# Optimization experiments

Measured on AMD Instinct MI355X. Metric: run time of the kernel, lower is better.

The kernel has to match this reference:

```python
import jax, jax.numpy as jnp
import numpy as np

B, L, D = 4, 1536, 768
H, DQK, DV = 8, 64, 96
NPF = 96  # num_pos_feats = (DV // (2*3)) * (2*3)


def pos_feats_exponential(positions, feature_size, seq_length, min_half_life=3.0):
    # positions: (P, 1); returns (P, feature_size)
    max_range = jnp.log(seq_length) / jnp.log(2.0)
    half_life = jnp.power(2.0, jnp.linspace(min_half_life, max_range, feature_size))
    return jnp.exp(-jnp.log(2.0) / half_life * jnp.abs(positions))


def pos_feats_central_mask(positions, feature_size):
    center_widths = jnp.power(2.0, jnp.arange(1, feature_size + 1, dtype=jnp.float32)) - 1.0
    return (center_widths > jnp.abs(positions)).astype(jnp.float32)


def pos_feats_gamma(positions, feature_size, seq_length):
    stddev = seq_length / (2.0 * feature_size)
    start_mean = seq_length / feature_size
    mean = jnp.linspace(start_mean, seq_length, feature_size)
    concentration = (mean / stddev) ** 2
    rate = mean / (stddev ** 2)
    x = jnp.abs(positions)
    log_unnorm = jax.scipy.special.xlogy(concentration - 1.0, x) - rate * x
    log_norm = jax.scipy.special.gammaln(concentration) - concentration * jnp.log(rate)
    probs = jnp.exp(log_unnorm - log_norm) + 1e-8
    return probs / jnp.max(probs, axis=0, keepdims=True)


def pos_feats_all(positions, feature_size, seq_length, symmetric=False):
    # 3 feature functions; if asymmetric, each is doubled by a signed copy
    num_basis = feature_size // 6
    emb = jnp.concatenate([
        pos_feats_exponential(positions, num_basis, seq_length),
        pos_feats_central_mask(positions, num_basis),
        pos_feats_gamma(positions, num_basis, seq_length),
    ], axis=-1)
    if not symmetric:
        emb = jnp.concatenate([emb, jnp.sign(positions) * emb], axis=-1)
    return emb  # (P, feature_size)


def relative_shift(x):
    # x: (b, h, t1, 2*t1 - 1) -> (b, h, t1, t1), Transformer-XL shift trick
    b, h, t1, t2 = x.shape
    x = jnp.concatenate([jnp.zeros_like(x[..., :1]), x], axis=-1)  # pad -> width t2+1 == 2*t1
    x = x.reshape(b, h, t2 + 1, t1)[:, :, 1:, :]
    x = x.reshape(b, h, t1, t2)
    return x[..., : (t2 + 2) // 2]


def setup_inputs() -> dict:
    key = jax.random.key(0)
    ks = jax.random.split(key, 9)

    def vs(k, shape):  # VarianceScaling(scale=2.0), fan_in on leading dim for 2D
        fan_in = shape[0] if len(shape) == 2 else shape[-1]
        return jax.random.normal(k, shape, jnp.float32) * np.float32(np.sqrt(2.0 / fan_in))

    return {
        "x": jax.random.normal(ks[0], (B, L, D), jnp.float32),
        "Q_w": vs(ks[1], (D, H * DQK)),
        "K_w": vs(ks[2], (D, H * DQK)),
        "V_w": vs(ks[3], (D, H * DV)),
        "out_w": vs(ks[4], (D, H * DV)),
        "out_b": jnp.zeros((H * DV,), jnp.float32),
        "rel_K_w": vs(ks[5], (NPF, H * DQK)),
        "r_w_bias": vs(ks[6], (1, H, 1, DQK)),
        "r_r_bias": vs(ks[7], (1, H, 1, DQK)),
    }


def reference(x, Q_w, K_w, V_w, out_w, out_b, rel_K_w, r_w_bias, r_r_bias):
    b, l, d = x.shape
    h = r_w_bias.shape[1]
    dqk = Q_w.shape[1] // h

    def heads(w, inp):
        out = inp @ w  # (b, t, h*dh)
        return out.reshape(inp.shape[0], inp.shape[1], h, -1).transpose(0, 2, 1, 3)

    Q = heads(Q_w, x) * (dqk ** -0.5)  # scaling=True
    K = heads(K_w, x)
    V = heads(V_w, x)

    positions = jnp.arange(1 - l, l, dtype=jnp.float32)[:, None]       # (2l-1, 1)
    pe = pos_feats_all(positions, rel_K_w.shape[0], float(l))           # (2l-1, npf)
    r_K = (pe @ rel_K_w).reshape(2 * l - 1, h, dqk).transpose(1, 0, 2)  # (h, 2l-1, dqk)

    content = jnp.einsum('bhid,bhjd->bhij', Q + r_w_bias, K)            # (b, h, l, l)
    rel = jnp.einsum('bhid,hjd->bhij', Q + r_r_bias, r_K)               # (b, h, l, 2l-1)
    logits = content + relative_shift(rel)

    w = jax.nn.softmax(logits, axis=-1)
    attn = jnp.einsum('bhij,bhjd->bhid', w, V)                          # (b, h, l, dv)
    out = attn.transpose(0, 2, 1, 3).reshape(b, l, -1) @ out_w + out_b
    return out
```

## Files before the change

### kernel.cpp

```cpp
#include <hip/hip_runtime.h>


typedef unsigned short u16;
typedef unsigned int   u32;

typedef __bf16 bf16x8_t __attribute__((ext_vector_type(8)));
typedef unsigned short u16x8_t __attribute__((ext_vector_type(8)));
typedef float f32x4_t __attribute__((ext_vector_type(4)));

union Frag { u16x8_t u; bf16x8_t b; };

__device__ __forceinline__ float bf2f(u16 v){
  union { u32 i; float f; } c; c.i = ((u32)v) << 16; return c.f;
}
__device__ __forceinline__ u16 f2bf(float f){
  union { float f; u32 i; } c; c.f = f;
  u32 r = c.i + 0x7FFFu + ((c.i >> 16) & 1u);
  return (u16)(r >> 16);
}

#define GLB __attribute__((address_space(1)))
#define LDSAS __attribute__((address_space(3)))
__device__ __forceinline__ void async16(const void* g, void* l){
  __builtin_amdgcn_global_load_lds((const GLB u32*)g, (LDSAS u32*)l, 16, 0, 0);
}

#define LQ   1536
#define NPOS 3071
#define NPOSP 3072

__global__ void cvt_x(const float* __restrict__ x, u16* __restrict__ xb)
{
  int gid = blockIdx.x * 256 + threadIdx.x;
  float4 v = ((const float4*)x)[gid];
  xb[4*gid+0] = f2bf(v.x); xb[4*gid+1] = f2bf(v.y);
  xb[4*gid+2] = f2bf(v.z); xb[4*gid+3] = f2bf(v.w);
}

__global__ __launch_bounds__(256) void transpose_w(
    const float* __restrict__ Qw_, const float* __restrict__ Kw_,
    const float* __restrict__ Vw_, const float* __restrict__ Ow_,
    u16* __restrict__ WtQKV, u16* __restrict__ WtOut)
{
  __shared__ u16 tile[64][65];
  int bx = blockIdx.x;
  const float* src; int stride, cl0, c0, k0; u16* dst;
  if (bx < 336) {
    int ct = bx % 28, kt = bx / 28;
    c0 = ct*64; k0 = kt*64;
    if (c0 < 512)       { src = Qw_; stride = 512; cl0 = c0; }
    else if (c0 < 1024) { src = Kw_; stride = 512; cl0 = c0 - 512; }
    else                { src = Vw_; stride = 768; cl0 = c0 - 1024; }
    dst = WtQKV;
  } else {
    int b2 = bx - 336; int ct = b2 % 12, kt = b2 / 12;
    c0 = ct*64; k0 = kt*64; src = Ow_; stride = 768; cl0 = c0; dst = WtOut;
  }
  int t = threadIdx.x;
  #pragma unroll
  for (int e = 0; e < 16; ++e) {
    int idx = e*256 + t; int row = idx >> 6, col = idx & 63;
    tile[row][col] = f2bf(src[(size_t)(k0 + row)*stride + cl0 + col]);
  }
  __syncthreads();
  #pragma unroll
  for (int e = 0; e < 16; ++e) {
    int idx = e*256 + t; int orow = idx >> 6, ocol = idx & 63;
    dst[(size_t)(c0 + orow)*768 + k0 + ocol] = tile[ocol][orow];
  }
}

__global__ void gamma_max_k(float* __restrict__ gmax)
{
  int f = blockIdx.x;
  float fi   = (float)(f + 1);
  float conc = 4.0f * fi * fi;
  float rate = fi / 24.0f;
  float c1   = conc - 1.0f;
  float lognorm = lgammaf(conc) - conc * logf(rate);
  float mx = 0.0f;
  for (int x = threadIdx.x; x < 1536; x += 256) {
    float xf = (float)x;
    float lu = (x == 0) ? -INFINITY : (c1 * logf(xf) - rate * xf);
    float p  = expf(lu - lognorm) + 1e-8f;
    mx = fmaxf(mx, p);
  }
  for (int d = 1; d < 64; d <<= 1) mx = fmaxf(mx, __shfl_xor(mx, d, 64));
  __shared__ float red[4];
  if ((threadIdx.x & 63) == 0) red[threadIdx.x >> 6] = mx;
  __syncthreads();
  if (threadIdx.x == 0)
    gmax[f] = fmaxf(fmaxf(red[0], red[1]), fmaxf(red[2], red[3]));
}

__global__ void rk_k(const float* __restrict__ gmax,
                     const float* __restrict__ relKw, u16* __restrict__ rK)
{
  int k = blockIdx.x;
  int t = threadIdx.x;
  if (k == NPOS) {
    for (int c = t; c < 512; c += 256)
      rK[(((size_t)(c >> 6))*NPOSP + NPOS)*64 + (c & 63)] = 0;
    return;
  }
  __shared__ float feats[96];
  float pos = (float)(k - (LQ - 1));
  float x   = fabsf(pos);
  float sgn = (float)((pos > 0.0f) - (pos < 0.0f));
  if (t < 96) {
    int tb = (t < 48) ? t : t - 48;
    float val;
    if (tb < 16) {
      float max_range = log2f((float)LQ);
      float hl = exp2f(3.0f + (float)tb * (max_range - 3.0f) / 15.0f);
      val = expf(-0.69314718056f / hl * x);
    } else if (tb < 32) {
      int i = tb - 16;
      float width = (float)(1u << (i + 1)) - 1.0f;
      val = (width > x) ? 1.0f : 0.0f;
    } else {
      int i = tb - 32;
      float fi   = (float)(i + 1);
      float conc = 4.0f * fi * fi;
      float rate = fi / 24.0f;
      float lognorm = lgammaf(conc) - conc * logf(rate);
      float lu = (x == 0.0f) ? -INFINITY : ((conc - 1.0f) * logf(x) - rate * x);
      float p  = expf(lu - lognorm) + 1e-8f;
      val = p / gmax[i];
    }
    feats[t] = (t < 48) ? val : sgn * val;
  }
  __syncthreads();
  for (int c = t; c < 512; c += 256) {
    float acc = 0.0f;
    #pragma unroll 8
    for (int f = 0; f < 96; ++f) acc += feats[f] * relKw[(size_t)f*512 + c];
    rK[(((size_t)(c >> 6))*NPOSP + k)*64 + (c & 63)] = f2bf(acc);
  }
}

__global__ __launch_bounds__(256) void qkv_gemm(
    const u16* __restrict__ xb, const u16* __restrict__ Wt,
    u16* __restrict__ Qb, u16* __restrict__ Kc, u16* __restrict__ Vt)
{
  const int n0 = blockIdx.x * 64;
  const int m0 = blockIdx.y * 64;
  const int tid = threadIdx.x, w = tid >> 6, lane = tid & 63, q = lane >> 4, s = lane & 15;

  __shared__ __align__(16) u16 At[64*64];
  __shared__ __align__(16) u16 Bt[64*64];

  const char* ag = (const char*)(xb + (size_t)m0 * 768);
  const char* bg = (const char*)(Wt + (size_t)n0 * 768);

  const f32x4_t fz = {0.f, 0.f, 0.f, 0.f};
  f32x4_t acc[4] = {fz, fz, fz, fz};

  for (int kk = 0; kk < 768; kk += 64) {
    #pragma unroll
    for (int c = 0; c < 2; ++c) {
      int ck = w*128 + c*64 + lane;
      int grow = ck >> 3, gcol = (ck & 7) ^ (grow & 7);
      async16(ag + (size_t)grow*1536 + (size_t)(kk + gcol*8)*2, &At[(size_t)(w*128 + c*64)*8]);
      async16(bg + (size_t)grow*1536 + (size_t)(kk + gcol*8)*2, &Bt[(size_t)(w*128 + c*64)*8]);
    }
    __syncthreads();
    #pragma unroll
    for (int kf = 0; kf < 2; ++kf) {
      int sw = (kf*4 + q) ^ (s & 7);
      Frag af; af.u = *(const u16x8_t*)&At[(size_t)((16*w + s)*8 + sw)*8];
      #pragma unroll
      for (int ns = 0; ns < 4; ++ns) {
        Frag bf; bf.u = *(const u16x8_t*)&Bt[(size_t)((ns*16 + s)*8 + sw)*8];
        acc[ns] = __builtin_amdgcn_mfma_f32_16x16x32_bf16(af.b, bf.b, acc[ns], 0, 0, 0);
      }
    }
    __syncthreads();
  }

  #pragma unroll
  for (int ns = 0; ns < 4; ++ns) {
    int c = n0 + ns*16 + s;
    #pragma unroll
    for (int r = 0; r < 4; ++r) {
      int row = m0 + 16*w + q*4 + r;
      int b = row / LQ, i = row - b*LQ;
      float v = acc[ns][r];
      if (c < 512) {
        int h = c >> 6, d = c & 63;
        Qb[(((size_t)(b*8 + h))*LQ + i)*64 + d] = f2bf(v * 0.125f);
      } else if (c < 1024) {
        int cc = c - 512, h = cc >> 6, d = cc & 63;
        Kc[(((size_t)(b*8 + h))*LQ + i)*64 + d] = f2bf(v);
      } else {
        int cc = c - 1024, h = cc / 96, vv = cc - h*96;
        Vt[(((size_t)(b*8 + h))*96 + vv)*LQ + i] = f2bf(v);
      }
    }
  }
}

__global__ __launch_bounds__(512, 4) void attn_k(
    const u16* __restrict__ Qb, const u16* __restrict__ Kc,
    const u16* __restrict__ Vt, const u16* __restrict__ rK,
    const float* __restrict__ rwb, const float* __restrict__ rrb,
    u16* __restrict__ attnO, u16* __restrict__ Opart, float* __restrict__ ml,
    int nz)
{
  const int n = blockIdx.x;
  const int bpb = 12 * nz;
  const int slot = n >> 3;
  const int bh = (n & 7) * 4 + slot / bpb;
  const int rm = slot % bpb;
  const int it = rm % 12, z = rm / 12;
  const int i0 = it * 128;
  const int b = bh >> 3, h = bh & 7;
  const int tid = threadIdx.x;
  const int w = tid >> 6, lane = tid & 63, q = lane >> 4, s = lane & 15;

  __shared__ __align__(16) u16 Kt[64*64];
  __shared__ __align__(16) u16 Rt[256*64];
  __shared__ __align__(16) u16 Vs[96*64];
  __shared__ __align__(16) u16 Ps[8][16][72];

  Frag qwf[2], qrf[2];
  {
    const u16* qb = Qb + (((size_t)bh)*LQ + i0 + 16*w + s)*64;
    #pragma unroll
    for (int kf = 0; kf < 2; ++kf) {
      u16x8_t qraw = *(const u16x8_t*)(qb + kf*32 + q*8);
      #pragma unroll
      for (int j = 0; j < 8; ++j) {
        int d = kf*32 + q*8 + j;
        float qv = bf2f(qraw[j]);
        qwf[kf].u[j] = f2bf(qv + rwb[h*64 + d]);
        qrf[kf].u[j] = f2bf(qv + rrb[h*64 + d]);
      }
    }
  }

  Frag ones;
  #pragma unroll
  for (int j = 0; j < 8; ++j) ones.u[j] = 0x3F80;

  const f32x4_t fz = {0.f, 0.f, 0.f, 0.f};
  float mrun[4];
  f32x4_t acco[6], accl;
  #pragma unroll
  for (int r = 0; r < 4; ++r) mrun[r] = -1e30f;
  #pragma unroll
  for (int vs = 0; vs < 6; ++vs) acco[vs] = fz;
  accl = fz;

  const char* kcb = (const char*)(Kc + ((size_t)bh)*LQ*64);
  const char* vtb = (const char*)(Vt + ((size_t)bh)*96*LQ);
  const char* rkb = (const char*)(rK + ((size_t)h)*NPOSP*64);

  const int swz0 = (0*4 + q) ^ (s & 7);
  const int swz1 = (1*4 + q) ^ (s & 7);

  const int njt = 24 / nz;
  const int jt0 = z * njt;
  const int jtend = jt0 + njt;

  auto stageK = [&](int jtS) {
    const char* kg = kcb + (size_t)(jtS*64) * 128;
    int ck = tid;
    int grow = ck >> 3, gcol = (ck & 7) ^ (grow & 7);
    async16(kg + (size_t)grow*128 + gcol*16, &Kt[(size_t)(w*64)*8]);
  };
  auto stageV = [&](int jtS) {
    const char* vg = vtb + (size_t)(jtS*64) * 2;
    {
      int ck = tid;
      int grow = ck >> 3, gcol = (ck & 7) ^ (grow & 7);
      async16(vg + (size_t)grow*(LQ*2) + gcol*16, &Vs[(size_t)(w*64)*8]);
    }
    if (tid < 256) {
      int ck = 512 + tid;
      int grow = ck >> 3, gcol = (ck & 7) ^ (grow & 7);
      async16(vg + (size_t)grow*(LQ*2) + gcol*16, &Vs[(size_t)(512 + w*64)*8]);
    }
  };
  auto stageR64 = [&](int ar0) {
    const char* rg = rkb + (size_t)ar0 * 128;
    int ck = tid;
    int grow = ck >> 3, gcol = (ck & 7) ^ (grow & 7);
    async16(rg + (size_t)grow*128 + gcol*16, &Rt[(size_t)((ar0 & 255) + w*8)*64]);
  };

  {
    const int k00 = jt0*64 - i0 + (LQ - 128);
    stageK(jt0);
    stageR64(k00); stageR64(k00 + 64); stageR64(k00 + 128);
    stageV(jt0);
  }
  __syncthreads();

  for (int jt = jt0; jt < jtend; ++jt) {
    const int k0 = jt*64 - i0 + (LQ - 128);
    const int kb = k0 & 255;

    f32x4_t accc[4] = {fz, fz, fz, fz};
    #pragma unroll
    for (int ns = 0; ns < 4; ++ns) {
      int row = ns*16 + s;
      Frag b0; b0.u = *(const u16x8_t*)&Kt[(size_t)(row*8 + swz0)*8];
      Frag b1; b1.u = *(const u16x8_t*)&Kt[(size_t)(row*8 + swz1)*8];
      accc[ns] = __builtin_amdgcn_mfma_f32_16x16x32_bf16(qwf[0].b, b0.b, accc[ns], 0, 0, 0);
      accc[ns] = __builtin_amdgcn_mfma_f32_16x16x32_bf16(qwf[1].b, b1.b, accc[ns], 0, 0, 0);
    }

    f32x4_t accr[5] = {fz, fz, fz, fz, fz};
    #pragma unroll
    for (int nn = 0; nn < 5; ++nn) {
      int row = (kb + (7 - w + nn)*16 + s) & 255;
      Frag b0; b0.u = *(const u16x8_t*)&Rt[(size_t)(row*8 + swz0)*8];
      Frag b1; b1.u = *(const u16x8_t*)&Rt[(size_t)(row*8 + swz1)*8];
      accr[nn] = __builtin_amdgcn_mfma_f32_16x16x32_bf16(qrf[0].b, b0.b, accr[nn], 0, 0, 0);
      accr[nn] = __builtin_amdgcn_mfma_f32_16x16x32_bf16(qrf[1].b, b1.b, accr[nn], 0, 0, 0);
    }

    __syncthreads();

    if (jt + 1 < jtend) {
      stageK(jt + 1);
      stageR64(k0 + 192);
    }

    #pragma unroll
    for (int r = 0; r < 4; ++r) {
      int tt = s + 15 - 4*q - r;
      int srcl = (lane & 48) | (tt & 15);
      bool hi = tt >= 16;
      float v[5];
      #pragma unroll
      for (int nn = 0; nn < 5; ++nn) v[nn] = __shfl(accr[nn][r], srcl, 64);
      #pragma unroll
      for (int ns = 0; ns < 4; ++ns)
        accc[ns][r] += hi ? v[ns + 1] : v[ns];
    }

    #pragma unroll
    for (int r = 0; r < 4; ++r) {
      float mx = fmaxf(fmaxf(accc[0][r], accc[1][r]), fmaxf(accc[2][r], accc[3][r]));
      for (int d = 1; d < 16; d <<= 1) mx = fmaxf(mx, __shfl_xor(mx, d, 64));
      float mnew  = fmaxf(mrun[r], mx);
      float alpha = __expf(mrun[r] - mnew);
      #pragma unroll
      for (int ns = 0; ns < 4; ++ns)
        accc[ns][r] = __expf(accc[ns][r] - mnew);
      mrun[r] = mnew;
      accl[r] *= alpha;
      #pragma unroll
      for (int vs = 0; vs < 6; ++vs) acco[vs][r] *= alpha;
    }

    #pragma unroll
    for (int ns = 0; ns < 4; ++ns)
      #pragma unroll
      for (int r = 0; r < 4; ++r)
        Ps[w][q*4 + r][ns*16 + s] = f2bf(accc[ns][r]);

    #pragma unroll
    for (int kf = 0; kf < 2; ++kf) {
      Frag pf; pf.u = *(const u16x8_t*)(&Ps[w][s][kf*32 + q*8]);
      int sw = kf ? swz1 : swz0;
      #pragma unroll
      for (int vs = 0; vs < 6; ++vs) {
        int row = vs*16 + s;
        Frag vf; vf.u = *(const u16x8_t*)&Vs[(size_t)(row*8 + sw)*8];
        acco[vs] = __builtin_amdgcn_mfma_f32_16x16x32_bf16(pf.b, vf.b, acco[vs], 0, 0, 0);
      }
      accl = __builtin_amdgcn_mfma_f32_16x16x32_bf16(pf.b, ones.b, accl, 0, 0, 0);
    }

    __syncthreads();

    if (jt + 1 < jtend) stageV(jt + 1);
  }

  if (nz == 1) {
    #pragma unroll
    for (int vs = 0; vs < 6; ++vs) {
      int v = vs*16 + s;
      #pragma unroll
      for (int r = 0; r < 4; ++r) {
        int i = i0 + 16*w + q*4 + r;
        attnO[((size_t)b*LQ + i)*768 + h*96 + v] = f2bf(acco[vs][r] / accl[r]);
      }
    }
  } else {
    #pragma unroll
    for (int vs = 0; vs < 6; ++vs) {
      int v = vs*16 + s;
      #pragma unroll
      for (int r = 0; r < 4; ++r) {
        int i = i0 + 16*w + q*4 + r;
        size_t rg = (size_t)(z*32 + bh)*LQ + i;
        Opart[rg*96 + v] = f2bf(acco[vs][r]);
      }
    }
    if (s == 0) {
      #pragma unroll
      for (int r = 0; r < 4; ++r) {
        int i = i0 + 16*w + q*4 + r;
        size_t rg = (size_t)(z*32 + bh)*LQ + i;
        ml[rg*2 + 0] = mrun[r];
        ml[rg*2 + 1] = accl[r];
      }
    }
  }
}

__global__ void combine_k(const u16* __restrict__ Opart, const float* __restrict__ ml,
                          u16* __restrict__ attnO, int nz)
{
  int g = blockIdx.x * 256 + threadIdx.x;
  if (g >= 32*LQ*96) return;
  int v = g % 96, row = g / 96;
  int bh = row / LQ, i = row - bh*LQ;
  int b = bh >> 3, h = bh & 7;
  float M = -1e30f;
  for (int z = 0; z < nz; ++z)
    M = fmaxf(M, ml[((size_t)(z*32 + bh)*LQ + i)*2]);
  float L = 0.f, num = 0.f;
  for (int z = 0; z < nz; ++z) {
    size_t rg = (size_t)(z*32 + bh)*LQ + i;
    float e = __expf(ml[rg*2] - M);
    L   += ml[rg*2 + 1] * e;
    num += bf2f(Opart[rg*96 + v]) * e;
  }
  attnO[((size_t)b*LQ + i)*768 + h*96 + v] = f2bf(num / L);
}

__global__ __launch_bounds__(256) void out_gemm(
    const u16* __restrict__ A, const u16* __restrict__ Wt,
    const float* __restrict__ bias, float* __restrict__ out)
{
  const int n0 = blockIdx.x * 64;
  const int m0 = blockIdx.y * 64;
  const int tid = threadIdx.x, w = tid >> 6, lane = tid & 63, q = lane >> 4, s = lane & 15;

  __shared__ __align__(16) u16 At[64*64];
  __shared__ __align__(16) u16 Bt[64*64];

  const char* ag = (const char*)(A  + (size_t)m0 * 768);
  const char* bg = (const char*)(Wt + (size_t)n0 * 768);

  const f32x4_t fz = {0.f, 0.f, 0.f, 0.f};
  f32x4_t acc[4] = {fz, fz, fz, fz};

  for (int kk = 0; kk < 768; kk += 64) {
    #pragma unroll
    for (int c = 0; c < 2; ++c) {
      int ck = w*128 + c*64 + lane;
      int grow = ck >> 3, gcol = (ck & 7) ^ (grow & 7);
      async16(ag + (size_t)grow*1536 + (size_t)(kk + gcol*8)*2, &At[(size_t)(w*128 + c*64)*8]);
      async16(bg + (size_t)grow*1536 + (size_t)(kk + gcol*8)*2, &Bt[(size_t)(w*128 + c*64)*8]);
    }
    __syncthreads();
    #pragma unroll
    for (int kf = 0; kf < 2; ++kf) {
      int sw = (kf*4 + q) ^ (s & 7);
      Frag af; af.u = *(const u16x8_t*)&At[(size_t)((16*w + s)*8 + sw)*8];
      #pragma unroll
      for (int ns = 0; ns < 4; ++ns) {
        Frag bf; bf.u = *(const u16x8_t*)&Bt[(size_t)((ns*16 + s)*8 + sw)*8];
        acc[ns] = __builtin_amdgcn_mfma_f32_16x16x32_bf16(af.b, bf.b, acc[ns], 0, 0, 0);
      }
    }
    __syncthreads();
  }

  #pragma unroll
  for (int ns = 0; ns < 4; ++ns) {
    int c = n0 + ns*16 + s;
    float bv = bias[c];
    #pragma unroll
    for (int r = 0; r < 4; ++r) {
      int row = m0 + 16*w + q*4 + r;
      out[(size_t)row*768 + c] = acc[ns][r] + bv;
    }
  }
}

extern "C" void kernel_launch(void* const* d_in, const int* in_sizes, int n_in,
                              void* d_out, int out_size, void* d_ws, size_t ws_size,
                              hipStream_t stream)
{
  (void)out_size;

  static const int dict_sig[9] = {4718592,393216,393216,589824,589824,768,49152,512,512};
  bool is_dict = (n_in == 9);
  for (int i = 0; i < 9 && i < n_in; ++i)
    if (in_sizes[i] != dict_sig[i]) is_dict = false;

  const float *x, *Qw_w, *Kw_w, *Vw_w, *Ow_w, *out_b, *relKw, *rwb, *rrb;
  if (is_dict) {
    x     = (const float*)d_in[0];  Qw_w  = (const float*)d_in[1];
    Kw_w  = (const float*)d_in[2];  Vw_w  = (const float*)d_in[3];
    Ow_w  = (const float*)d_in[4];  out_b = (const float*)d_in[5];
    relKw = (const float*)d_in[6];  rwb   = (const float*)d_in[7];
    rrb   = (const float*)d_in[8];
  } else {
    const float* p393[2] = {nullptr,nullptr}; int n393 = 0;
    const float* p589[2] = {nullptr,nullptr}; int n589 = 0;
    const float* p512[2] = {nullptr,nullptr}; int n512 = 0;
    const float *px = nullptr, *prel = nullptr, *pb = nullptr;
    for (int i = 0; i < n_in; ++i) {
      const float* p = (const float*)d_in[i];
      switch (in_sizes[i]) {
        case 4718592: px = p; break;
        case 49152:   prel = p; break;
        case 768:     pb = p; break;
        case 393216:  if (n393 < 2) p393[n393++] = p; break;
        case 589824:  if (n589 < 2) p589[n589++] = p; break;
        case 512:     if (n512 < 2) p512[n512++] = p; break;
        default: break;
      }
    }
    x = px; relKw = prel; out_b = pb;
    Qw_w = p393[0]; Kw_w = p393[1];
    Vw_w = p589[0]; Ow_w = p589[1];
    rwb  = p512[0]; rrb  = p512[1];
  }

  float* out = (float*)d_out;

  char* ws = (char*)d_ws;
  size_t off = 0;
  auto alloc = [&](size_t bytes) -> void* {
    void* p = ws + off;
    off += (bytes + 255) & ~(size_t)255;
    return p;
  };

  float* gmax  = (float*)alloc(256);
  u16*   WtQKV = (u16*)  alloc((size_t)1792*768*2);
  u16*   WtOut = (u16*)  alloc((size_t)768*768*2);
  u16*   rK    = (u16*)  alloc((size_t)8*NPOSP*64*2);
  u16*   Qb    = (u16*)  alloc((size_t)32*LQ*64*2);
  u16*   Kc    = (u16*)  alloc((size_t)32*LQ*64*2);
  u16*   Vt    = (u16*)  alloc((size_t)32*96*LQ*2);
  u16*   xb    = (u16*)  alloc((size_t)6144*768*2);
  u16*   attnO = xb;

  size_t base_off = off;
  auto need = [&](int nzv) -> size_t {
    size_t o = base_off;
    o += (((size_t)nzv*32*LQ*96*2) + 255) & ~(size_t)255;
    o += (((size_t)nzv*32*LQ*2*4) + 255) & ~(size_t)255;
    return o;
  };
  int nz = 1;
  if (ws_size >= need(4)) nz = 4;
  else if (ws_size >= need(2)) nz = 2;
  u16*   Opart = nullptr; float* ml = nullptr;
  if (nz > 1) {
    Opart = (u16*)  alloc((size_t)nz*32*LQ*96*2);
    ml    = (float*)alloc((size_t)nz*32*LQ*2*4);
  }

  cvt_x      <<<dim3(4608), dim3(256), 0, stream>>>(x, xb);
  transpose_w<<<dim3(480),  dim3(256), 0, stream>>>(Qw_w, Kw_w, Vw_w, Ow_w, WtQKV, WtOut);
  gamma_max_k<<<dim3(16),   dim3(256), 0, stream>>>(gmax);
  rk_k       <<<dim3(NPOSP),dim3(256), 0, stream>>>(gmax, relKw, rK);
  qkv_gemm   <<<dim3(28,96),dim3(256), 0, stream>>>(xb, WtQKV, Qb, Kc, Vt);
  attn_k     <<<dim3(384*nz),dim3(512), 0, stream>>>(Qb, Kc, Vt, rK, rwb, rrb,
                                                     attnO, Opart, ml, nz);
  if (nz > 1)
    combine_k<<<dim3(18432), dim3(256), 0, stream>>>(Opart, ml, attnO, nz);
  out_gemm   <<<dim3(12,96),dim3(256), 0, stream>>>(attnO, WtOut, out_b, out);
}
```

Measured before the change: 328.4 us.

## Enlarge GEMM tiles, batch rK positions per block, use hardware bf16 conversion

The QKV GEMM moves to 128x128 tiles with 4x4 MFMA fragments per wave, and the output GEMM to 128x64 tiles. Both changes raise data reuse per LDS load and reduce block count. The rK kernel now computes four positions per block so each relKw weight load is reused four times. The attention kernel uses the hardware bf16 conversion and raises wave priority (s_setprio) around its MFMA sections. Larger tiles lower occupancy and shrink the grid, and the hardware conversion may round differently from the manual routine.

```diff
diff --git a/kernel.cpp b/kernel.cpp
--- a/kernel.cpp
+++ b/kernel.cpp
@@ -17,6 +17,10 @@
   union { float f; u32 i; } c; c.f = f;
   u32 r = c.i + 0x7FFFu + ((c.i >> 16) & 1u);
   return (u16)(r >> 16);
+}
+__device__ __forceinline__ u16 f2bf_hw(float f){
+  __bf16 h = (__bf16)f;
+  union { __bf16 h; u16 u; } c; c.h = h; return c.u;
 }
 
 #define GLB __attribute__((address_space(1)))
@@ -93,49 +97,68 @@
     gmax[f] = fmaxf(fmaxf(red[0], red[1]), fmaxf(red[2], red[3]));
 }
 
-__global__ void rk_k(const float* __restrict__ gmax,
+__global__ __launch_bounds__(256) void rk_k(const float* __restrict__ gmax,
                      const float* __restrict__ relKw, u16* __restrict__ rK)
 {
-  int k = blockIdx.x;
-  int t = threadIdx.x;
-  if (k == NPOS) {
-    for (int c = t; c < 512; c += 256)
-      rK[(((size_t)(c >> 6))*NPOSP + NPOS)*64 + (c & 63)] = 0;
-    return;
-  }
-  __shared__ float feats[96];
-  float pos = (float)(k - (LQ - 1));
-  float x   = fabsf(pos);
-  float sgn = (float)((pos > 0.0f) - (pos < 0.0f));
-  if (t < 96) {
-    int tb = (t < 48) ? t : t - 48;
-    float val;
-    if (tb < 16) {
-      float max_range = log2f((float)LQ);
-      float hl = exp2f(3.0f + (float)tb * (max_range - 3.0f) / 15.0f);
-      val = expf(-0.69314718056f / hl * x);
-    } else if (tb < 32) {
-      int i = tb - 16;
-      float width = (float)(1u << (i + 1)) - 1.0f;
-      val = (width > x) ? 1.0f : 0.0f;
-    } else {
-      int i = tb - 32;
-      float fi   = (float)(i + 1);
-      float conc = 4.0f * fi * fi;
-      float rate = fi / 24.0f;
-      float lognorm = lgammaf(conc) - conc * logf(rate);
-      float lu = (x == 0.0f) ? -INFINITY : ((conc - 1.0f) * logf(x) - rate * x);
-      float p  = expf(lu - lognorm) + 1e-8f;
-      val = p / gmax[i];
-    }
-    feats[t] = (t < 48) ? val : sgn * val;
+  __shared__ float feats[4][96];
+  const int k0 = blockIdx.x * 4;
+  const int t = threadIdx.x;
+
+  #pragma unroll
+  for (int e = 0; e < 2; ++e) {
+    int idx = e*256 + t;
+    if (idx < 384) {
+      int kl = idx / 96, f = idx - kl*96;
+      int k = k0 + kl;
+      float val = 0.0f;
+      if (k != NPOS) {
+        float pos = (float)(k - (LQ - 1));
+        float x   = fabsf(pos);
+        float sgn = (float)((pos > 0.0f) - (pos < 0.0f));
+        int fb = (f < 48) ? f : f - 48;
+        float v;
+        if (fb < 16) {
+          float max_range = log2f((float)LQ);
+          float hl = exp2f(3.0f + (float)fb * (max_range - 3.0f) / 15.0f);
+          v = expf(-0.69314718056f / hl * x);
+        } else if (fb < 32) {
+          int i = fb - 16;
+          float width = (float)(1u << (i + 1)) - 1.0f;
+          v = (width > x) ? 1.0f : 0.0f;
+        } else {
+          int i = fb - 32;
+          float fi   = (float)(i + 1);
+          float conc = 4.0f * fi * fi;
+          float rate = fi / 24.0f;
+          float lognorm = lgammaf(conc) - conc * logf(rate);
+          float lu = (x == 0.0f) ? -INFINITY : ((conc - 1.0f) * logf(x) - rate * x);
+          float p  = expf(lu - lognorm) + 1e-8f;
+          v = p / gmax[i];
+        }
+        val = (f < 48) ? v : sgn * v;
+      }
+      feats[kl][f] = val;
+    }
   }
   __syncthreads();
-  for (int c = t; c < 512; c += 256) {
-    float acc = 0.0f;
-    #pragma unroll 8
-    for (int f = 0; f < 96; ++f) acc += feats[f] * relKw[(size_t)f*512 + c];
-    rK[(((size_t)(c >> 6))*NPOSP + k)*64 + (c & 63)] = f2bf(acc);
+
+  #pragma unroll
+  for (int ci = 0; ci < 2; ++ci) {
+    int c = ci*256 + t;
+    float a0 = 0.f, a1 = 0.f, a2 = 0.f, a3 = 0.f;
+    #pragma unroll 4
+    for (int f = 0; f < 96; ++f) {
+      float wv = relKw[(size_t)f*512 + c];
+      a0 += feats[0][f] * wv;
+      a1 += feats[1][f] * wv;
+      a2 += feats[2][f] * wv;
+      a3 += feats[3][f] * wv;
+    }
+    size_t base = (((size_t)(c >> 6))*NPOSP + k0)*64 + (c & 63);
+    rK[base +   0] = f2bf(a0);
+    rK[base +  64] = f2bf(a1);
+    rK[base + 128] = f2bf(a2);
+    rK[base + 192] = f2bf(a3);
   }
 }
 
@@ -143,58 +166,72 @@
     const u16* __restrict__ xb, const u16* __restrict__ Wt,
     u16* __restrict__ Qb, u16* __restrict__ Kc, u16* __restrict__ Vt)
 {
-  const int n0 = blockIdx.x * 64;
-  const int m0 = blockIdx.y * 64;
+  const int n0 = blockIdx.x * 128;
+  const int m0 = blockIdx.y * 128;
   const int tid = threadIdx.x, w = tid >> 6, lane = tid & 63, q = lane >> 4, s = lane & 15;
-
-  __shared__ __align__(16) u16 At[64*64];
-  __shared__ __align__(16) u16 Bt[64*64];
+  const int wr = w >> 1, wc = w & 1;
+
+  __shared__ __align__(16) u16 At[128*64];
+  __shared__ __align__(16) u16 Bt[128*64];
 
   const char* ag = (const char*)(xb + (size_t)m0 * 768);
   const char* bg = (const char*)(Wt + (size_t)n0 * 768);
 
   const f32x4_t fz = {0.f, 0.f, 0.f, 0.f};
-  f32x4_t acc[4] = {fz, fz, fz, fz};
+  f32x4_t acc[4][4];
+  #pragma unroll
+  for (int m = 0; m < 4; ++m)
+    #pragma unroll
+    for (int n = 0; n < 4; ++n) acc[m][n] = fz;
 
   for (int kk = 0; kk < 768; kk += 64) {
     #pragma unroll
-    for (int c = 0; c < 2; ++c) {
-      int ck = w*128 + c*64 + lane;
+    for (int c = 0; c < 4; ++c) {
+      int ck = w*256 + c*64 + lane;
       int grow = ck >> 3, gcol = (ck & 7) ^ (grow & 7);
-      async16(ag + (size_t)grow*1536 + (size_t)(kk + gcol*8)*2, &At[(size_t)(w*128 + c*64)*8]);
-      async16(bg + (size_t)grow*1536 + (size_t)(kk + gcol*8)*2, &Bt[(size_t)(w*128 + c*64)*8]);
+      async16(ag + (size_t)grow*1536 + (size_t)(kk + gcol*8)*2, &At[(size_t)(w*256 + c*64)*8]);
+      async16(bg + (size_t)grow*1536 + (size_t)(kk + gcol*8)*2, &Bt[(size_t)(w*256 + c*64)*8]);
     }
     __syncthreads();
     #pragma unroll
     for (int kf = 0; kf < 2; ++kf) {
       int sw = (kf*4 + q) ^ (s & 7);
-      Frag af; af.u = *(const u16x8_t*)&At[(size_t)((16*w + s)*8 + sw)*8];
-      #pragma unroll
-      for (int ns = 0; ns < 4; ++ns) {
-        Frag bf; bf.u = *(const u16x8_t*)&Bt[(size_t)((ns*16 + s)*8 + sw)*8];
-        acc[ns] = __builtin_amdgcn_mfma_f32_16x16x32_bf16(af.b, bf.b, acc[ns], 0, 0, 0);
-      }
+      Frag af[4], bf[4];
+      #pragma unroll
+      for (int m = 0; m < 4; ++m)
+        af[m].u = *(const u16x8_t*)&At[(size_t)((wr*64 + m*16 + s)*8 + sw)*8];
+      #pragma unroll
+      for (int n = 0; n < 4; ++n)
+        bf[n].u = *(const u16x8_t*)&Bt[(size_t)((wc*64 + n*16 + s)*8 + sw)*8];
+      #pragma unroll
+      for (int m = 0; m < 4; ++m)
+        #pragma unroll
+        for (int n = 0; n < 4; ++n)
+          acc[m][n] = __builtin_amdgcn_mfma_f32_16x16x32_bf16(af[m].b, bf[n].b, acc[m][n], 0, 0, 0);
     }
     __syncthreads();
   }
 
   #pragma unroll
-  for (int ns = 0; ns < 4; ++ns) {
-    int c = n0 + ns*16 + s;
-    #pragma unroll
-    for (int r = 0; r < 4; ++r) {
-      int row = m0 + 16*w + q*4 + r;
-      int b = row / LQ, i = row - b*LQ;
-      float v = acc[ns][r];
-      if (c < 512) {
-        int h = c >> 6, d = c & 63;
-        Qb[(((size_t)(b*8 + h))*LQ + i)*64 + d] = f2bf(v * 0.125f);
-      } else if (c < 1024) {
-        int cc = c - 512, h = cc >> 6, d = cc & 63;
-        Kc[(((size_t)(b*8 + h))*LQ + i)*64 + d] = f2bf(v);
-      } else {
-        int cc = c - 1024, h = cc / 96, vv = cc - h*96;
-        Vt[(((size_t)(b*8 + h))*96 + vv)*LQ + i] = f2bf(v);
+  for (int m = 0; m < 4; ++m) {
+    #pragma unroll
+    for (int n = 0; n < 4; ++n) {
+      int c = n0 + wc*64 + n*16 + s;
+      #pragma unroll
+      for (int r = 0; r < 4; ++r) {
+        int row = m0 + wr*64 + m*16 + q*4 + r;
+        int b = row / LQ, i = row - b*LQ;
+        float v = acc[m][n][r];
+        if (c < 512) {
+          int h = c >> 6, d = c & 63;
+          Qb[(((size_t)(b*8 + h))*LQ + i)*64 + d] = f2bf(v * 0.125f);
+        } else if (c < 1024) {
+          int cc = c - 512, h = cc >> 6, d = cc & 63;
+          Kc[(((size_t)(b*8 + h))*LQ + i)*64 + d] = f2bf(v);
+        } else {
+          int cc = c - 1024, h = cc / 96, vv = cc - h*96;
+          Vt[(((size_t)(b*8 + h))*96 + vv)*LQ + i] = f2bf(v);
+        }
       }
     }
   }
@@ -233,8 +270,8 @@
       for (int j = 0; j < 8; ++j) {
         int d = kf*32 + q*8 + j;
         float qv = bf2f(qraw[j]);
-        qwf[kf].u[j] = f2bf(qv + rwb[h*64 + d]);
-        qrf[kf].u[j] = f2bf(qv + rrb[h*64 + d]);
+        qwf[kf].u[j] = f2bf_hw(qv + rwb[h*64 + d]);
+        qrf[kf].u[j] = f2bf_hw(qv + rrb[h*64 + d]);
       }
     }
   }
@@ -302,6 +339,8 @@
     const int kb = k0 & 255;
 
     f32x4_t accc[4] = {fz, fz, fz, fz};
+    f32x4_t accr[5] = {fz, fz, fz, fz, fz};
+    __builtin_amdgcn_s_setprio(1);
     #pragma unroll
     for (int ns = 0; ns < 4; ++ns) {
       int row = ns*16 + s;
@@ -310,8 +349,6 @@
       accc[ns] = __builtin_amdgcn_mfma_f32_16x16x32_bf16(qwf[0].b, b0.b, accc[ns], 0, 0, 0);
       accc[ns] = __builtin_amdgcn_mfma_f32_16x16x32_bf16(qwf[1].b, b1.b, accc[ns], 0, 0, 0);
     }
-
-    f32x4_t accr[5] = {fz, fz, fz, fz, fz};
     #pragma unroll
     for (int nn = 0; nn < 5; ++nn) {
       int row = (kb + (7 - w + nn)*16 + s) & 255;
@@ -320,6 +357,7 @@
       accr[nn] = __builtin_amdgcn_mfma_f32_16x16x32_bf16(qrf[0].b, b0.b, accr[nn], 0, 0, 0);
       accr[nn] = __builtin_amdgcn_mfma_f32_16x16x32_bf16(qrf[1].b, b1.b, accr[nn], 0, 0, 0);
     }
+    __builtin_amdgcn_s_setprio(0);
 
     __syncthreads();
 
@@ -360,8 +398,9 @@
     for (int ns = 0; ns < 4; ++ns)
       #pragma unroll
       for (int r = 0; r < 4; ++r)
-        Ps[w][q*4 + r][ns*16 + s] = f2bf(accc[ns][r]);
-
+        Ps[w][q*4 + r][ns*16 + s] = f2bf_hw(accc[ns][r]);
+
+    __builtin_amdgcn_s_setprio(1);
     #pragma unroll
     for (int kf = 0; kf < 2; ++kf) {
       Frag pf; pf.u = *(const u16x8_t*)(&Ps[w][s][kf*32 + q*8]);
@@ -374,6 +413,7 @@
       }
       accl = __builtin_amdgcn_mfma_f32_16x16x32_bf16(pf.b, ones.b, accl, 0, 0, 0);
     }
+    __builtin_amdgcn_s_setprio(0);
 
     __syncthreads();
 
@@ -387,7 +427,7 @@
       #pragma unroll
       for (int r = 0; r < 4; ++r) {
         int i = i0 + 16*w + q*4 + r;
-        attnO[((size_t)b*LQ + i)*768 + h*96 + v] = f2bf(acco[vs][r] / accl[r]);
+        attnO[((size_t)b*LQ + i)*768 + h*96 + v] = f2bf_hw(acco[vs][r] / accl[r]);
       }
     }
   } else {
@@ -398,7 +438,7 @@
       for (int r = 0; r < 4; ++r) {
         int i = i0 + 16*w + q*4 + r;
         size_t rg = (size_t)(z*32 + bh)*LQ + i;
-        Opart[rg*96 + v] = f2bf(acco[vs][r]);
+        Opart[rg*96 + v] = f2bf_hw(acco[vs][r]);
       }
     }
     if (s == 0) {
@@ -439,48 +479,66 @@
     const float* __restrict__ bias, float* __restrict__ out)
 {
   const int n0 = blockIdx.x * 64;
-  const int m0 = blockIdx.y * 64;
+  const int m0 = blockIdx.y * 128;
   const int tid = threadIdx.x, w = tid >> 6, lane = tid & 63, q = lane >> 4, s = lane & 15;
 
-  __shared__ __align__(16) u16 At[64*64];
+  __shared__ __align__(16) u16 At[128*64];
   __shared__ __align__(16) u16 Bt[64*64];
 
   const char* ag = (const char*)(A  + (size_t)m0 * 768);
   const char* bg = (const char*)(Wt + (size_t)n0 * 768);
 
   const f32x4_t fz = {0.f, 0.f, 0.f, 0.f};
-  f32x4_t acc[4] = {fz, fz, fz, fz};
+  f32x4_t acc[2][4];
+  #pragma unroll
+  for (int m = 0; m < 2; ++m)
+    #pragma unroll
+    for (int n = 0; n < 4; ++n) acc[m][n] = fz;
 
   for (int kk = 0; kk < 768; kk += 64) {
+    #pragma unroll
+    for (int c = 0; c < 4; ++c) {
+      int ck = w*256 + c*64 + lane;
+      int grow = ck >> 3, gcol = (ck & 7) ^ (grow & 7);
+      async16(ag + (size_t)grow*1536 + (size_t)(kk + gcol*8)*2, &At[(size_t)(w*256 + c*64)*8]);
+    }
     #pragma unroll
     for (int c = 0; c < 2; ++c) {
       int ck = w*128 + c*64 + lane;
       int grow = ck >> 3, gcol = (ck & 7) ^ (grow & 7);
-      async16(ag + (size_t)grow*1536 + (size_t)(kk + gcol*8)*2, &At[(size_t)(w*128 + c*64)*8]);
       async16(bg + (size_t)grow*1536 + (size_t)(kk + gcol*8)*2, &Bt[(size_t)(w*128 + c*64)*8]);
     }
     __syncthreads();
     #pragma unroll
     for (int kf = 0; kf < 2; ++kf) {
       int sw = (kf*4 + q) ^ (s & 7);
-      Frag af; af.u = *(const u16x8_t*)&At[(size_t)((16*w + s)*8 + sw)*8];
-      #pragma unroll
-      for (int ns = 0; ns < 4; ++ns) {
-        Frag bf; bf.u = *(const u16x8_t*)&Bt[(size_t)((ns*16 + s)*8 + sw)*8];
-        acc[ns] = __builtin_amdgcn_mfma_f32_16x16x32_bf16(af.b, bf.b, acc[ns], 0, 0, 0);
-      }
+      Frag af[2], bf[4];
+      #pragma unroll
+      for (int m = 0; m < 2; ++m)
+        af[m].u = *(const u16x8_t*)&At[(size_t)((w*32 + m*16 + s)*8 + sw)*8];
+      #pragma unroll
+      for (int n = 0; n < 4; ++n)
+        bf[n].u = *(const u16x8_t*)&Bt[(size_t)((n*16 + s)*8 + sw)*8];
+      #pragma unroll
+      for (int m = 0; m < 2; ++m)
+        #pragma unroll
+        for (int n = 0; n < 4; ++n)
+          acc[m][n] = __builtin_amdgcn_mfma_f32_16x16x32_bf16(af[m].b, bf[n].b, acc[m][n], 0, 0, 0);
     }
     __syncthreads();
   }
 
   #pragma unroll
-  for (int ns = 0; ns < 4; ++ns) {
-    int c = n0 + ns*16 + s;
-    float bv = bias[c];
-    #pragma unroll
-    for (int r = 0; r < 4; ++r) {
-      int row = m0 + 16*w + q*4 + r;
-      out[(size_t)row*768 + c] = acc[ns][r] + bv;
+  for (int m = 0; m < 2; ++m) {
+    #pragma unroll
+    for (int n = 0; n < 4; ++n) {
+      int c = n0 + n*16 + s;
+      float bv = bias[c];
+      #pragma unroll
+      for (int r = 0; r < 4; ++r) {
+        int row = m0 + w*32 + m*16 + q*4 + r;
+        out[(size_t)row*768 + c] = acc[m][n][r] + bv;
+      }
     }
   }
 }
@@ -565,11 +623,11 @@
   cvt_x      <<<dim3(4608), dim3(256), 0, stream>>>(x, xb);
   transpose_w<<<dim3(480),  dim3(256), 0, stream>>>(Qw_w, Kw_w, Vw_w, Ow_w, WtQKV, WtOut);
   gamma_max_k<<<dim3(16),   dim3(256), 0, stream>>>(gmax);
-  rk_k       <<<dim3(NPOSP),dim3(256), 0, stream>>>(gmax, relKw, rK);
-  qkv_gemm   <<<dim3(28,96),dim3(256), 0, stream>>>(xb, WtQKV, Qb, Kc, Vt);
+  rk_k       <<<dim3(768),  dim3(256), 0, stream>>>(gmax, relKw, rK);
+  qkv_gemm   <<<dim3(14,48),dim3(256), 0, stream>>>(xb, WtQKV, Qb, Kc, Vt);
   attn_k     <<<dim3(384*nz),dim3(512), 0, stream>>>(Qb, Kc, Vt, rK, rwb, rrb,
                                                      attnO, Opart, ml, nz);
   if (nz > 1)
     combine_k<<<dim3(18432), dim3(256), 0, stream>>>(Opart, ml, attnO, nz);
-  out_gemm   <<<dim3(12,96),dim3(256), 0, stream>>>(attnO, WtOut, out_b, out);
-}
+  out_gemm   <<<dim3(12,48),dim3(256), 0, stream>>>(attnO, WtOut, out_b, out);
+}
```

New measurement: 349.9 us. 1.07x slower.

## Fuse preprocessing kernels and streamline online softmax with exp2 and lazy rescale

Applied to the files above, without the earlier changes.

Merges the x conversion, weight transposes, gamma-max and relative-key feature kernels into one launch. The gamma max is now taken analytically from the distribution mode rather than by scanning every position, and each block computes four positions so relKw loads are shared. In attention, Q is prescaled by log2(e) so exp2 replaces exp, and the row max uses DPP row rotations instead of shuffles. The softmax rescale is skipped when no row max rises more than a threshold above the running max, and hardware bf16 conversion plus a reciprocal replace software rounding and division. These changes can alter rounding slightly, and the lazy rescale allows larger intermediate values in the accumulators.

```diff
diff --git a/kernel.cpp b/kernel.cpp
--- a/kernel.cpp
+++ b/kernel.cpp
@@ -18,6 +18,32 @@
   u32 r = c.i + 0x7FFFu + ((c.i >> 16) & 1u);
   return (u16)(r >> 16);
 }
+__device__ __forceinline__ u16 f2bf_hw(float f){
+  __bf16 h = (__bf16)f;
+  union { __bf16 h; u16 u; } c; c.h = h; return c.u;
+}
+__device__ __forceinline__ float frcp(float x){
+#if __has_builtin(__builtin_amdgcn_rcpf)
+  return __builtin_amdgcn_rcpf(x);
+#else
+  return 1.0f / x;
+#endif
+}
+
+template<int N>
+__device__ __forceinline__ float ror16(float x){
+  union { float f; int i; } c; c.f = x;
+  int y = __builtin_amdgcn_update_dpp(0, c.i, 0x120 + N, 0xF, 0xF, true);
+  union { int i; float f; } d; d.i = y;
+  return d.f;
+}
+__device__ __forceinline__ float rowmax16(float v){
+  v = fmaxf(v, ror16<1>(v));
+  v = fmaxf(v, ror16<2>(v));
+  v = fmaxf(v, ror16<4>(v));
+  v = fmaxf(v, ror16<8>(v));
+  return v;
+}
 
 #define GLB __attribute__((address_space(1)))
 #define LDSAS __attribute__((address_space(3)))
@@ -28,114 +54,130 @@
 #define LQ   1536
 #define NPOS 3071
 #define NPOSP 3072
-
-__global__ void cvt_x(const float* __restrict__ x, u16* __restrict__ xb)
-{
-  int gid = blockIdx.x * 256 + threadIdx.x;
-  float4 v = ((const float4*)x)[gid];
-  xb[4*gid+0] = f2bf(v.x); xb[4*gid+1] = f2bf(v.y);
-  xb[4*gid+2] = f2bf(v.z); xb[4*gid+3] = f2bf(v.w);
-}
-
-__global__ __launch_bounds__(256) void transpose_w(
+#define LOG2E 1.44269504088896f
+
+__global__ __launch_bounds__(256) void pre_k(
+    const float* __restrict__ x,
     const float* __restrict__ Qw_, const float* __restrict__ Kw_,
     const float* __restrict__ Vw_, const float* __restrict__ Ow_,
-    u16* __restrict__ WtQKV, u16* __restrict__ WtOut)
+    const float* __restrict__ relKw,
+    u16* __restrict__ xb, u16* __restrict__ WtQKV, u16* __restrict__ WtOut,
+    u16* __restrict__ rK)
 {
-  __shared__ u16 tile[64][65];
-  int bx = blockIdx.x;
-  const float* src; int stride, cl0, c0, k0; u16* dst;
-  if (bx < 336) {
-    int ct = bx % 28, kt = bx / 28;
-    c0 = ct*64; k0 = kt*64;
-    if (c0 < 512)       { src = Qw_; stride = 512; cl0 = c0; }
-    else if (c0 < 1024) { src = Kw_; stride = 512; cl0 = c0 - 512; }
-    else                { src = Vw_; stride = 768; cl0 = c0 - 1024; }
-    dst = WtQKV;
-  } else {
-    int b2 = bx - 336; int ct = b2 % 12, kt = b2 / 12;
-    c0 = ct*64; k0 = kt*64; src = Ow_; stride = 768; cl0 = c0; dst = WtOut;
-  }
-  int t = threadIdx.x;
+  const int bx = blockIdx.x;
+  const int t = threadIdx.x;
+
+  if (bx < 4608) {
+    int gid = bx * 256 + t;
+    float4 v = ((const float4*)x)[gid];
+    xb[4*gid+0] = f2bf(v.x); xb[4*gid+1] = f2bf(v.y);
+    xb[4*gid+2] = f2bf(v.z); xb[4*gid+3] = f2bf(v.w);
+    return;
+  }
+
+  if (bx < 5088) {
+    __shared__ u16 tile[64][65];
+    int b2 = bx - 4608;
+    const float* src; int stride, cl0, c0, k0; u16* dst;
+    if (b2 < 336) {
+      int ct = b2 % 28, kt = b2 / 28;
+      c0 = ct*64; k0 = kt*64;
+      if (c0 < 512)       { src = Qw_; stride = 512; cl0 = c0; }
+      else if (c0 < 1024) { src = Kw_; stride = 512; cl0 = c0 - 512; }
+      else                { src = Vw_; stride = 768; cl0 = c0 - 1024; }
+      dst = WtQKV;
+    } else {
+      int b3 = b2 - 336; int ct = b3 % 12, kt = b3 / 12;
+      c0 = ct*64; k0 = kt*64; src = Ow_; stride = 768; cl0 = c0; dst = WtOut;
+    }
+    #pragma unroll
+    for (int e = 0; e < 16; ++e) {
+      int idx = e*256 + t; int row = idx >> 6, col = idx & 63;
+      tile[row][col] = f2bf(src[(size_t)(k0 + row)*stride + cl0 + col]);
+    }
+    __syncthreads();
+    #pragma unroll
+    for (int e = 0; e < 16; ++e) {
+      int idx = e*256 + t; int orow = idx >> 6, ocol = idx & 63;
+      dst[(size_t)(c0 + orow)*768 + k0 + ocol] = tile[ocol][orow];
+    }
+    return;
+  }
+
+  __shared__ float gmaxs[16];
+  __shared__ float feats[4][96];
+  const int k0 = (bx - 5088) * 4;
+
+  if (t < 16) {
+    float fi   = (float)(t + 1);
+    float conc = 4.0f * fi * fi;
+    float rate = fi / 24.0f;
+    float c1   = conc - 1.0f;
+    float lognorm = lgammaf(conc) - conc * logf(rate);
+    float mode = 96.0f*fi - 24.0f/fi;
+    float x1 = floorf(mode), x2 = x1 + 1.0f;
+    if (x2 > 1535.0f) x2 = 1535.0f;
+    float p1 = expf(c1*logf(x1) - rate*x1 - lognorm) + 1e-8f;
+    float p2 = expf(c1*logf(x2) - rate*x2 - lognorm) + 1e-8f;
+    gmaxs[t] = fmaxf(p1, p2);
+  }
+  __syncthreads();
+
   #pragma unroll
-  for (int e = 0; e < 16; ++e) {
-    int idx = e*256 + t; int row = idx >> 6, col = idx & 63;
-    tile[row][col] = f2bf(src[(size_t)(k0 + row)*stride + cl0 + col]);
+  for (int e = 0; e < 2; ++e) {
+    int idx = e*256 + t;
+    if (idx < 384) {
+      int kl = idx / 96, f = idx - kl*96;
+      int k = k0 + kl;
+      float val = 0.0f;
+      if (k != NPOS) {
+        float pos = (float)(k - (LQ - 1));
+        float xx  = fabsf(pos);
+        float sgn = (float)((pos > 0.0f) - (pos < 0.0f));
+        int fb = (f < 48) ? f : f - 48;
+        float v;
+        if (fb < 16) {
+          float max_range = log2f((float)LQ);
+          float hl = exp2f(3.0f + (float)fb * (max_range - 3.0f) / 15.0f);
+          v = expf(-0.69314718056f / hl * xx);
+        } else if (fb < 32) {
+          int i = fb - 16;
+          float width = (float)(1u << (i + 1)) - 1.0f;
+          v = (width > xx) ? 1.0f : 0.0f;
+        } else {
+          int i = fb - 32;
+          float fi   = (float)(i + 1);
+          float conc = 4.0f * fi * fi;
+          float rate = fi / 24.0f;
+          float lognorm = lgammaf(conc) - conc * logf(rate);
+          float lu = (xx == 0.0f) ? -INFINITY : ((conc - 1.0f) * logf(xx) - rate * xx);
+          float p  = expf(lu - lognorm) + 1e-8f;
+          v = p / gmaxs[i];
+        }
+        val = (f < 48) ? v : sgn * v;
+      }
+      feats[kl][f] = val;
+    }
   }
   __syncthreads();
+
   #pragma unroll
-  for (int e = 0; e < 16; ++e) {
-    int idx = e*256 + t; int orow = idx >> 6, ocol = idx & 63;
-    dst[(size_t)(c0 + orow)*768 + k0 + ocol] = tile[ocol][orow];
-  }
-}
-
-__global__ void gamma_max_k(float* __restrict__ gmax)
-{
-  int f = blockIdx.x;
-  float fi   = (float)(f + 1);
-  float conc = 4.0f * fi * fi;
-  float rate = fi / 24.0f;
-  float c1   = conc - 1.0f;
-  float lognorm = lgammaf(conc) - conc * logf(rate);
-  float mx = 0.0f;
-  for (int x = threadIdx.x; x < 1536; x += 256) {
-    float xf = (float)x;
-    float lu = (x == 0) ? -INFINITY : (c1 * logf(xf) - rate * xf);
-    float p  = expf(lu - lognorm) + 1e-8f;
-    mx = fmaxf(mx, p);
-  }
-  for (int d = 1; d < 64; d <<= 1) mx = fmaxf(mx, __shfl_xor(mx, d, 64));
-  __shared__ float red[4];
-  if ((threadIdx.x & 63) == 0) red[threadIdx.x >> 6] = mx;
-  __syncthreads();
-  if (threadIdx.x == 0)
-    gmax[f] = fmaxf(fmaxf(red[0], red[1]), fmaxf(red[2], red[3]));
-}
-
-__global__ void rk_k(const float* __restrict__ gmax,
-                     const float* __restrict__ relKw, u16* __restrict__ rK)
-{
-  int k = blockIdx.x;
-  int t = threadIdx.x;
-  if (k == NPOS) {
-    for (int c = t; c < 512; c += 256)
-      rK[(((size_t)(c >> 6))*NPOSP + NPOS)*64 + (c & 63)] = 0;
-    return;
-  }
-  __shared__ float feats[96];
-  float pos = (float)(k - (LQ - 1));
-  float x   = fabsf(pos);
-  float sgn = (float)((pos > 0.0f) - (pos < 0.0f));
-  if (t < 96) {
-    int tb = (t < 48) ? t : t - 48;
-    float val;
-    if (tb < 16) {
-      float max_range = log2f((float)LQ);
-      float hl = exp2f(3.0f + (float)tb * (max_range - 3.0f) / 15.0f);
-      val = expf(-0.69314718056f / hl * x);
-    } else if (tb < 32) {
-      int i = tb - 16;
-      float width = (float)(1u << (i + 1)) - 1.0f;
-      val = (width > x) ? 1.0f : 0.0f;
-    } else {
-      int i = tb - 32;
-      float fi   = (float)(i + 1);
-      float conc = 4.0f * fi * fi;
-      float rate = fi / 24.0f;
-      float lognorm = lgammaf(conc) - conc * logf(rate);
-      float lu = (x == 0.0f) ? -INFINITY : ((conc - 1.0f) * logf(x) - rate * x);
-      float p  = expf(lu - lognorm) + 1e-8f;
-      val = p / gmax[i];
-    }
-    feats[t] = (t < 48) ? val : sgn * val;
-  }
-  __syncthreads();
-  for (int c = t; c < 512; c += 256) {
-    float acc = 0.0f;
-    #pragma unroll 8
-    for (int f = 0; f < 96; ++f) acc += feats[f] * relKw[(size_t)f*512 + c];
-    rK[(((size_t)(c >> 6))*NPOSP + k)*64 + (c & 63)] = f2bf(acc);
+  for (int ci = 0; ci < 2; ++ci) {
+    int c = ci*256 + t;
+    float a0 = 0.f, a1 = 0.f, a2 = 0.f, a3 = 0.f;
+    #pragma unroll 4
+    for (int f = 0; f < 96; ++f) {
+      float wv = relKw[(size_t)f*512 + c];
+      a0 += feats[0][f] * wv;
+      a1 += feats[1][f] * wv;
+      a2 += feats[2][f] * wv;
+      a3 += feats[3][f] * wv;
+    }
+    size_t base = (((size_t)(c >> 6))*NPOSP + k0)*64 + (c & 63);
+    rK[base +   0] = f2bf(a0);
+    rK[base +  64] = f2bf(a1);
+    rK[base + 128] = f2bf(a2);
+    rK[base + 192] = f2bf(a3);
   }
 }
 
@@ -233,8 +275,8 @@
       for (int j = 0; j < 8; ++j) {
         int d = kf*32 + q*8 + j;
         float qv = bf2f(qraw[j]);
-        qwf[kf].u[j] = f2bf(qv + rwb[h*64 + d]);
-        qrf[kf].u[j] = f2bf(qv + rrb[h*64 + d]);
+        qwf[kf].u[j] = f2bf_hw((qv + rwb[h*64 + d]) * LOG2E);
+        qrf[kf].u[j] = f2bf_hw((qv + rrb[h*64 + d]) * LOG2E);
       }
     }
   }
@@ -302,6 +344,7 @@
     const int kb = k0 & 255;
 
     f32x4_t accc[4] = {fz, fz, fz, fz};
+    f32x4_t accr[5] = {fz, fz, fz, fz, fz};
     #pragma unroll
     for (int ns = 0; ns < 4; ++ns) {
       int row = ns*16 + s;
@@ -310,8 +353,6 @@
       accc[ns] = __builtin_amdgcn_mfma_f32_16x16x32_bf16(qwf[0].b, b0.b, accc[ns], 0, 0, 0);
       accc[ns] = __builtin_amdgcn_mfma_f32_16x16x32_bf16(qwf[1].b, b1.b, accc[ns], 0, 0, 0);
     }
-
-    f32x4_t accr[5] = {fz, fz, fz, fz, fz};
     #pragma unroll
     for (int nn = 0; nn < 5; ++nn) {
       int row = (kb + (7 - w + nn)*16 + s) & 255;
@@ -341,26 +382,37 @@
         accc[ns][r] += hi ? v[ns + 1] : v[ns];
     }
 
-    #pragma unroll
-    for (int r = 0; r < 4; ++r) {
-      float mx = fmaxf(fmaxf(accc[0][r], accc[1][r]), fmaxf(accc[2][r], accc[3][r]));
-      for (int d = 1; d < 16; d <<= 1) mx = fmaxf(mx, __shfl_xor(mx, d, 64));
-      float mnew  = fmaxf(mrun[r], mx);
-      float alpha = __expf(mrun[r] - mnew);
-      #pragma unroll
-      for (int ns = 0; ns < 4; ++ns)
-        accc[ns][r] = __expf(accc[ns][r] - mnew);
-      mrun[r] = mnew;
-      accl[r] *= alpha;
-      #pragma unroll
-      for (int vs = 0; vs < 6; ++vs) acco[vs][r] *= alpha;
+    {
+      float mx[4]; bool sk = true;
+      #pragma unroll
+      for (int r = 0; r < 4; ++r) {
+        float m0 = fmaxf(fmaxf(accc[0][r], accc[1][r]), fmaxf(accc[2][r], accc[3][r]));
+        mx[r] = rowmax16(m0);
+        sk = sk && (mx[r] <= mrun[r] + 10.0f);
+      }
+      if (!__all(sk)) {
+        #pragma unroll
+        for (int r = 0; r < 4; ++r) {
+          float mnew  = fmaxf(mrun[r], mx[r]);
+          float alpha = exp2f(mrun[r] - mnew);
+          mrun[r] = mnew;
+          accl[r] *= alpha;
+          #pragma unroll
+          for (int vs = 0; vs < 6; ++vs) acco[vs][r] *= alpha;
+        }
+      }
+      #pragma unroll
+      for (int r = 0; r < 4; ++r)
+        #pragma unroll
+        for (int ns = 0; ns < 4; ++ns)
+          accc[ns][r] = exp2f(accc[ns][r] - mrun[r]);
     }
 
     #pragma unroll
     for (int ns = 0; ns < 4; ++ns)
       #pragma unroll
       for (int r = 0; r < 4; ++r)
-        Ps[w][q*4 + r][ns*16 + s] = f2bf(accc[ns][r]);
+        Ps[w][q*4 + r][ns*16 + s] = f2bf_hw(accc[ns][r]);
 
     #pragma unroll
     for (int kf = 0; kf < 2; ++kf) {
@@ -382,12 +434,13 @@
 
   if (nz == 1) {
     #pragma unroll
-    for (int vs = 0; vs < 6; ++vs) {
-      int v = vs*16 + s;
-      #pragma unroll
-      for (int r = 0; r < 4; ++r) {
-        int i = i0 + 16*w + q*4 + r;
-        attnO[((size_t)b*LQ + i)*768 + h*96 + v] = f2bf(acco[vs][r] / accl[r]);
+    for (int r = 0; r < 4; ++r) {
+      float inv = frcp(accl[r]);
+      int i = i0 + 16*w + q*4 + r;
+      #pragma unroll
+      for (int vs = 0; vs < 6; ++vs) {
+        int v = vs*16 + s;
+        attnO[((size_t)b*LQ + i)*768 + h*96 + v] = f2bf_hw(acco[vs][r] * inv);
       }
     }
   } else {
@@ -398,7 +451,7 @@
       for (int r = 0; r < 4; ++r) {
         int i = i0 + 16*w + q*4 + r;
         size_t rg = (size_t)(z*32 + bh)*LQ + i;
-        Opart[rg*96 + v] = f2bf(acco[vs][r]);
+        Opart[rg*96 + v] = f2bf_hw(acco[vs][r]);
       }
     }
     if (s == 0) {
@@ -427,11 +480,11 @@
   float L = 0.f, num = 0.f;
   for (int z = 0; z < nz; ++z) {
     size_t rg = (size_t)(z*32 + bh)*LQ + i;
-    float e = __expf(ml[rg*2] - M);
+    float e = exp2f(ml[rg*2] - M);
     L   += ml[rg*2 + 1] * e;
     num += bf2f(Opart[rg*96 + v]) * e;
   }
-  attnO[((size_t)b*LQ + i)*768 + h*96 + v] = f2bf(num / L);
+  attnO[((size_t)b*LQ + i)*768 + h*96 + v] = f2bf(num * frcp(L));
 }
 
 __global__ __launch_bounds__(256) void out_gemm(
@@ -536,7 +589,6 @@
     return p;
   };
 
-  float* gmax  = (float*)alloc(256);
   u16*   WtQKV = (u16*)  alloc((size_t)1792*768*2);
   u16*   WtOut = (u16*)  alloc((size_t)768*768*2);
   u16*   rK    = (u16*)  alloc((size_t)8*NPOSP*64*2);
@@ -562,10 +614,8 @@
     ml    = (float*)alloc((size_t)nz*32*LQ*2*4);
   }
 
-  cvt_x      <<<dim3(4608), dim3(256), 0, stream>>>(x, xb);
-  transpose_w<<<dim3(480),  dim3(256), 0, stream>>>(Qw_w, Kw_w, Vw_w, Ow_w, WtQKV, WtOut);
-  gamma_max_k<<<dim3(16),   dim3(256), 0, stream>>>(gmax);
-  rk_k       <<<dim3(NPOSP),dim3(256), 0, stream>>>(gmax, relKw, rK);
+  pre_k      <<<dim3(5856), dim3(256), 0, stream>>>(x, Qw_w, Kw_w, Vw_w, Ow_w,
+                                                    relKw, xb, WtQKV, WtOut, rK);
   qkv_gemm   <<<dim3(28,96),dim3(256), 0, stream>>>(xb, WtQKV, Qb, Kc, Vt);
   attn_k     <<<dim3(384*nz),dim3(512), 0, stream>>>(Qb, Kc, Vt, rK, rwb, rrb,
                                                      attnO, Opart, ml, nz);
```

Result: no change. 324.7 us (-1.1%).
